# Kernel tuning notes

Measured on AMD Instinct MI355X. Metric: run time of the kernel, lower is better.

## Reference

```python
import jax, jax.numpy as jnp
import numpy as np

B, A, D, H, F = 256, 96, 384, 192, 96   # molecules, atoms, feat, hidden, species-MLP out
S = 4                                   # number of species (H, C, N, O)
E = B * A * 32                          # edges (avg degree 32)
CUTOFF = 5.2


def smooth_cutoff(d, cutoff):
    # Smoothstep-style cutoff: 1 at d=0, smoothly -> 0 at d=cutoff (Smoothstep class, reversed edges)
    x = jnp.clip((cutoff - d) / cutoff, 0.0, 1.0)
    return x ** 3 * (x * (6.0 * x - 15.0) + 10.0)


def setup_inputs() -> dict:
    key = jax.random.key(0)
    ks = jax.random.split(key, 9)
    species = jax.random.randint(ks[0], (B, A), 0, S, dtype=jnp.int32)
    in_features = jax.random.normal(ks[1], (B, A, D), dtype=jnp.float32)
    atom_index12 = jax.random.randint(ks[2], (2, E), 0, B * A, dtype=jnp.int32)
    distances = jax.random.uniform(ks[3], (E,), jnp.float32, 0.1, CUTOFF)
    total_charges = jnp.zeros((B,), jnp.float32)
    W1 = jax.random.normal(ks[4], (S, D, H), jnp.float32) / np.float32(np.sqrt(D))
    W2 = jax.random.normal(ks[5], (S, H, F), jnp.float32) / np.float32(np.sqrt(H))
    Wn = jax.random.normal(ks[6], (S, F, F), jnp.float32) / np.float32(np.sqrt(F))
    Wf = jax.random.normal(ks[7], (S, 2 * F, 1), jnp.float32) / np.float32(np.sqrt(2 * F))
    return dict(species=species, in_features=in_features, atom_index12=atom_index12,
                distances=distances, total_charges=total_charges,
                W1=W1, W2=W2, Wn=Wn, Wf=Wf,
                decay_prefactor=jnp.asarray(1.0, jnp.float32),
                decay_factor=jnp.asarray(1.0, jnp.float32))


def reference(species, in_features, atom_index12, distances, total_charges,
              W1, W2, Wn, Wf, decay_prefactor, decay_factor):
    b, a, d = in_features.shape
    n = b * a
    sp = species.reshape(-1)                      # [N]
    x = in_features.reshape(n, d)                 # [N, D]

    # per-species main MLP dispatch: internal[i] = MLP_{sp[i]}(x[i])
    internal = jnp.zeros((n, F), x.dtype)
    for s in range(S):
        mask = (sp == s)[:, None]
        h = jax.nn.gelu(x @ W1[s]) @ W2[s]        # [N, F]
        internal = internal + jnp.where(mask, h, jnp.zeros((), x.dtype))

    # per-species neighbor MLP
    nbr = jnp.zeros((n, F), x.dtype)
    for s in range(S):
        mask = (sp == s)[:, None]
        nbr = nbr + jnp.where(mask, internal @ Wn[s], jnp.zeros((), x.dtype))

    # distance-decayed edge messages: merged[i0] += nbr[i1]*w, merged[i1] += nbr[i0]*w
    decay = (decay_prefactor ** 2) * jnp.exp(-(decay_factor ** 2) * distances) \
            * smooth_cutoff(distances, CUTOFF)    # [E]
    i0, i1 = atom_index12[0], atom_index12[1]
    m_to_i0 = nbr[i1] * decay[:, None]            # [E, F]
    m_to_i1 = nbr[i0] * decay[:, None]
    merged = jax.ops.segment_sum(jnp.concatenate([m_to_i0, m_to_i1], axis=0),
                                 jnp.concatenate([i0, i1], axis=0),
                                 num_segments=n)  # [N, F]

    feats = jnp.concatenate([internal, merged], axis=-1)  # [N, 2F]

    # per-species final head -> precharges
    precharges = jnp.zeros((n,), x.dtype)
    for s in range(S):
        mask = (sp == s)
        precharges = precharges + jnp.where(mask, (feats @ Wf[s])[:, 0], jnp.zeros((), x.dtype))
    precharges = precharges.reshape(b, a)

    # total-charge redistribution (uniform factors, no learned redistribution)
    dummy_mask = species != -1
    factors = 1.0 / dummy_mask.sum(-1, keepdims=True).astype(x.dtype)
    charges = precharges + (total_charges - precharges.sum(-1))[:, None] * factors
    charges = jnp.where(dummy_mask, charges, jnp.zeros((), x.dtype))
    return species, charges, precharges
```

## Files before the change

### kernel.cpp

```cpp
#include <hip/hip_runtime.h>
#include <cstdint>
#include <cstddef>

#define NBm 256
#define NAm 96
#define NDm 384
#define NHm 192
#define NFm 96
#define NSm 4
#define NATOMS (NBm*NAm)
#define NEe (NATOMS*32)
#define NMSG (2*NEe)
#define HBLK 1536
#define CUTOFF_ 5.2f

typedef __attribute__((ext_vector_type(8))) short short8;
typedef __attribute__((ext_vector_type(4))) float float4v;
typedef __attribute__((ext_vector_type(2))) int int2v;

__device__ __forceinline__ short f2bf(float f){
  union { float f; unsigned u; } v; v.f = f;
  unsigned r = v.u + 0x7FFFu + ((v.u >> 16) & 1u);
  return (short)(r >> 16);
}

__device__ __forceinline__ float gelu_t(float x){
  float u = 0.7978845608028654f * (x + 0.044715f * x*x*x);
  float e = __expf(-2.0f * fabsf(u));
  float t = (1.0f - e) / (1.0f + e);
  t = (u >= 0.f) ? t : -t;
  return 0.5f * x * (1.0f + t);
}

__global__ void k_zero4(int* __restrict__ spc){
  if (threadIdx.x < NSm) spc[threadIdx.x] = 0;
}

__global__ void k_spcount(const int* __restrict__ sp, int* __restrict__ spc){
  __shared__ int h[NSm];
  int t = threadIdx.x;
  if (t < NSm) h[t] = 0;
  __syncthreads();
  int i = blockIdx.x*256 + t;
  atomicAdd(&h[sp[i]], 1);
  __syncthreads();
  if (t < NSm) atomicAdd(&spc[t], h[t]);
}

__global__ void k_spscan(const int* __restrict__ spc, int* __restrict__ sps, int* __restrict__ spcur){
  if (threadIdx.x==0 && blockIdx.x==0){
    int r=0;
    for (int s=0;s<NSm;s++){ sps[s]=r; spcur[s]=r; r+=spc[s]; }
    sps[NSm]=r;
  }
}

__global__ void k_spscatter(const int* __restrict__ sp, int* __restrict__ spcur,
                            int* __restrict__ order){
  __shared__ int h[NSm], base[NSm];
  int t = threadIdx.x;
  if (t < NSm) h[t]=0;
  __syncthreads();
  int i = blockIdx.x*256 + t;
  int s = sp[i];
  int lr = atomicAdd(&h[s], 1);
  __syncthreads();
  if (t < NSm) base[t] = atomicAdd(&spcur[t], h[t]);
  __syncthreads();
  order[base[s] + lr] = i;
}

#define W1N (NSm*NDm*NHm)
#define W2N (NSm*NHm*NFm)
#define WNN (NSm*NFm*NFm)
__global__ void k_wprep(const float* __restrict__ W1, const float* __restrict__ W2,
                        const float* __restrict__ Wn,
                        short* __restrict__ W1t, short* __restrict__ W2t,
                        short* __restrict__ Wnt){
  int idx = blockIdx.x*256 + threadIdx.x;
  if (idx < W1N){
    int s = idx / (NDm*NHm); int rem = idx - s*NDm*NHm;
    int k = rem / NHm, c = rem - k*NHm;
    W1t[(s*NHm + c)*NDm + k] = f2bf(W1[idx]);
  } else if (idx < W1N + W2N){
    int j = idx - W1N;
    int s = j / (NHm*NFm); int rem = j - s*NHm*NFm;
    int k = rem / NFm, c = rem - k*NFm;
    W2t[(s*NFm + c)*NHm + k] = f2bf(W2[j]);
  } else if (idx < W1N + W2N + WNN){
    int j = idx - W1N - W2N;
    int s = j / (NFm*NFm); int rem = j - s*NFm*NFm;
    int k = rem / NFm, c = rem - k*NFm;
    Wnt[(s*NFm + c)*NFm + k] = f2bf(Wn[j]);
  }
}

__global__ void k_xprep(const float* __restrict__ X, short* __restrict__ Xb){
  int i = (blockIdx.x*256 + threadIdx.x) * 8;
  float4v a = *(const float4v*)(X + i);
  float4v b = *(const float4v*)(X + i + 4);
  short8 o;
  o[0]=f2bf(a[0]); o[1]=f2bf(a[1]); o[2]=f2bf(a[2]); o[3]=f2bf(a[3]);
  o[4]=f2bf(b[0]); o[5]=f2bf(b[1]); o[6]=f2bf(b[2]); o[7]=f2bf(b[3]);
  *(short8*)(Xb + i) = o;
}

__global__ __launch_bounds__(256) void k_mlp(
    const short* __restrict__ Xb, const int* __restrict__ order,
    const int* __restrict__ sps,
    const short* __restrict__ W1t, const short* __restrict__ W2t,
    const short* __restrict__ Wnt,
    float* __restrict__ internal_g, float* __restrict__ nbr_g){
  const int s = blockIdx.y;
  const int s0 = sps[s];
  const int cnt = sps[s+1] - s0;
  const int row0 = blockIdx.x * 64;
  if (row0 >= cnt) return;

  __shared__ short Hs[64][200];
  __shared__ short Ws[192*40];
  __shared__ short Is[64][104];
  __shared__ int aids[64];

  const int tid = threadIdx.x;
  if (tid < 64){
    int r = row0 + tid;
    aids[tid] = order[s0 + ((r < cnt) ? r : 0)];
  }
  __syncthreads();

  const int wave = tid >> 6, lane = tid & 63;
  const int lrow = lane & 15, quad = lane >> 4;
  const int arow = wave*16 + lrow;
  const short* xrow = Xb + (size_t)aids[arow]*NDm + quad*8;

  short8 afs[12];
  #pragma unroll
  for (int kb=0; kb<12; kb++) afs[kb] = *(const short8*)(xrow + kb*32);

  const short* W1s = W1t + (size_t)s*NHm*NDm;
  float4v acc[12];
  #pragma unroll
  for (int i=0;i<12;i++){ acc[i][0]=0.f; acc[i][1]=0.f; acc[i][2]=0.f; acc[i][3]=0.f; }

  for (int kb=0; kb<12; kb++){
    __syncthreads();
    for (int e = tid; e < 192*4; e += 256){
      int c = e >> 2, kq = (e & 3) * 8;
      *(short8*)(&Ws[c*40 + kq]) = *(const short8*)(W1s + c*NDm + kb*32 + kq);
    }
    __syncthreads();
    short8 af = afs[kb];
    #pragma unroll
    for (int ct=0; ct<12; ct++){
      short8 bfb = *(const short8*)(&Ws[(ct*16 + lrow)*40 + quad*8]);
      acc[ct] = __builtin_amdgcn_mfma_f32_16x16x32_bf16(af, bfb, acc[ct], 0,0,0);
    }
  }
  #pragma unroll
  for (int ct=0; ct<12; ct++){
    #pragma unroll
    for (int r=0;r<4;r++){
      Hs[wave*16 + quad*4 + r][ct*16 + lrow] = f2bf(gelu_t(acc[ct][r]));
    }
  }

  const short* W2s = W2t + (size_t)s*NFm*NHm;
  float4v acc2[6];
  #pragma unroll
  for (int i=0;i<6;i++){ acc2[i][0]=0.f; acc2[i][1]=0.f; acc2[i][2]=0.f; acc2[i][3]=0.f; }
  for (int kb=0; kb<6; kb++){
    __syncthreads();
    for (int e = tid; e < 96*4; e += 256){
      int c = e >> 2, kq = (e & 3) * 8;
      *(short8*)(&Ws[c*40 + kq]) = *(const short8*)(W2s + c*NHm + kb*32 + kq);
    }
    __syncthreads();
    short8 af2 = *(const short8*)(&Hs[wave*16 + lrow][kb*32 + quad*8]);
    #pragma unroll
    for (int ct=0; ct<6; ct++){
      short8 bfb = *(const short8*)(&Ws[(ct*16 + lrow)*40 + quad*8]);
      acc2[ct] = __builtin_amdgcn_mfma_f32_16x16x32_bf16(af2, bfb, acc2[ct], 0,0,0);
    }
  }
  #pragma unroll
  for (int ct=0; ct<6; ct++){
    #pragma unroll
    for (int r=0;r<4;r++){
      int row = wave*16 + quad*4 + r, col = ct*16 + lrow;
      float v = acc2[ct][r];
      if (row0 + row < cnt) internal_g[(size_t)aids[row]*NFm + col] = v;
      Is[row][col] = f2bf(v);
    }
  }

  const short* Wns = Wnt + (size_t)s*NFm*NFm;
  float4v acc3[6];
  #pragma unroll
  for (int i=0;i<6;i++){ acc3[i][0]=0.f; acc3[i][1]=0.f; acc3[i][2]=0.f; acc3[i][3]=0.f; }
  for (int kb=0; kb<3; kb++){
    __syncthreads();
    for (int e = tid; e < 96*4; e += 256){
      int c = e >> 2, kq = (e & 3) * 8;
      *(short8*)(&Ws[c*40 + kq]) = *(const short8*)(Wns + c*NFm + kb*32 + kq);
    }
    __syncthreads();
    short8 af3 = *(const short8*)(&Is[wave*16 + lrow][kb*32 + quad*8]);
    #pragma unroll
    for (int ct=0; ct<6; ct++){
      short8 bfb = *(const short8*)(&Ws[(ct*16 + lrow)*40 + quad*8]);
      acc3[ct] = __builtin_amdgcn_mfma_f32_16x16x32_bf16(af3, bfb, acc3[ct], 0,0,0);
    }
  }
  #pragma unroll
  for (int ct=0; ct<6; ct++){
    #pragma unroll
    for (int r=0;r<4;r++){
      int row = wave*16 + quad*4 + r, col = ct*16 + lrow;
      if (row0 + row < cnt) nbr_g[(size_t)aids[row]*NFm + col] = acc3[ct][r];
    }
  }
}

__global__ void k_nd4(const float* __restrict__ internal, const float* __restrict__ nbr,
                      const int* __restrict__ sp, const float* __restrict__ Wf,
                      float* __restrict__ pre, float* __restrict__ nd4){
  int a = blockIdx.x*4 + (threadIdx.x >> 6);
  int lane = threadIdx.x & 63;
  bool lo = lane < 32;
  const float* ip = internal + (size_t)a*NFm;
  const float* np = nbr + (size_t)a*NFm;
  float iv1 = ip[lane],            nv1 = np[lane];
  float iv2 = lo ? ip[64+lane]:0.f, nv2 = lo ? np[64+lane]:0.f;
  int s = sp[a];
  const float* wfs = Wf + s*2*NFm;
  float d = iv1*wfs[lane] + (lo ? iv2*wfs[64+lane] : 0.f);
  float n0, n1, n2, n3;
  {
    const float* w0 = Wf + 0*2*NFm + NFm;
    const float* w1 = Wf + 1*2*NFm + NFm;
    const float* w2 = Wf + 2*2*NFm + NFm;
    const float* w3 = Wf + 3*2*NFm + NFm;
    n0 = nv1*w0[lane] + (lo ? nv2*w0[64+lane] : 0.f);
    n1 = nv1*w1[lane] + (lo ? nv2*w1[64+lane] : 0.f);
    n2 = nv1*w2[lane] + (lo ? nv2*w2[64+lane] : 0.f);
    n3 = nv1*w3[lane] + (lo ? nv2*w3[64+lane] : 0.f);
  }
  #pragma unroll
  for (int m=1; m<64; m<<=1){
    d  += __shfl_xor(d,  m, 64);
    n0 += __shfl_xor(n0, m, 64);
    n1 += __shfl_xor(n1, m, 64);
    n2 += __shfl_xor(n2, m, 64);
    n3 += __shfl_xor(n3, m, 64);
  }
  if (lane == 0){
    pre[a] = d;
    float4v v; v[0]=n0; v[1]=n1; v[2]=n2; v[3]=n3;
    *(float4v*)(nd4 + (size_t)a*4) = v;
  }
}

__global__ __launch_bounds__(1024) void k_hist(const int* __restrict__ ai,
                                               int* __restrict__ Hist){
  __shared__ int h[NBm];
  int t = threadIdx.x;
  if (t < NBm) h[t] = 0;
  __syncthreads();
  int m = blockIdx.x*1024 + t;
  int mol = ai[m] / NAm;
  atomicAdd(&h[mol], 1);
  __syncthreads();
  if (t < NBm) Hist[blockIdx.x*NBm + t] = h[t];
}

__global__ void k_mscan(int* __restrict__ Hist, int* __restrict__ Tot){
  __shared__ int sums[256];
  int mol = blockIdx.x, t = threadIdx.x;
  int v[6]; int loc = 0;
  #pragma unroll
  for (int j=0;j<6;j++){ v[j] = Hist[(t*6+j)*NBm + mol]; loc += v[j]; }
  sums[t] = loc; __syncthreads();
  for (int off=1; off<256; off<<=1){
    int x = (t >= off) ? sums[t-off] : 0;
    __syncthreads();
    sums[t] += x;
    __syncthreads();
  }
  int run = sums[t] - loc;
  #pragma unroll
  for (int j=0;j<6;j++){ Hist[(t*6+j)*NBm + mol] = run; run += v[j]; }
  if (t == 255) Tot[mol] = run;
}

__global__ void k_segscan(const int* __restrict__ Tot, int* __restrict__ Seg){
  __shared__ int s[256];
  int t = threadIdx.x;
  int v = Tot[t]; s[t] = v; __syncthreads();
  for (int off=1; off<256; off<<=1){
    int x = (t >= off) ? s[t-off] : 0;
    __syncthreads();
    s[t] += x;
    __syncthreads();
  }
  Seg[t] = s[t] - v;
  if (t == 255) Seg[256] = s[255];
}

__global__ __launch_bounds__(1024) void k_scatter(const int* __restrict__ ai,
    const float* __restrict__ dist, const float* __restrict__ pref,
    const float* __restrict__ fac, const int* __restrict__ Hist,
    const int* __restrict__ Seg, int2v* __restrict__ Msg){
  __shared__ int cnt[NBm];
  __shared__ int off[NBm];
  int t = threadIdx.x;
  if (t < NBm){ cnt[t] = 0; off[t] = Seg[t] + Hist[blockIdx.x*NBm + t]; }
  __syncthreads();
  int m = blockIdx.x*1024 + t;
  int dest = ai[m];
  int other = ai[(m < NEe) ? m + NEe : m - NEe];
  int e = (m < NEe) ? m : m - NEe;
  float d = dist[e];
  float x = (CUTOFF_ - d) * (1.0f/CUTOFF_);
  x = fminf(fmaxf(x, 0.f), 1.f);
  float sc = x*x*x*(x*(6.f*x - 15.f) + 10.f);
  float p = pref[0], fc = fac[0];
  float w = p*p * expf(-fc*fc*d) * sc;
  int mol = dest / NAm, dl = dest - mol*NAm;
  int rank = atomicAdd(&cnt[mol], 1);
  int2v msg; msg[0] = (other << 7) | dl; msg[1] = __float_as_int(w);
  Msg[off[mol] + rank] = msg;
}

__global__ __launch_bounds__(256) void k_accum(const int* __restrict__ Seg,
    const int2v* __restrict__ Msg, const float* __restrict__ nd4,
    const int* __restrict__ sp, const float* __restrict__ pre,
    const float* __restrict__ tc, float* __restrict__ out){
  __shared__ float acc[NAm];
  __shared__ int spl[NAm];
  __shared__ float red[128];
  int mol = blockIdx.x, t = threadIdx.x;
  if (t < NAm){ acc[t] = 0.f; spl[t] = sp[mol*NAm + t]; }
  __syncthreads();
  int s0 = Seg[mol], s1 = Seg[mol+1];
  for (int i = s0 + t; i < s1; i += 256){
    int2v kw = Msg[i];
    int key = kw[0]; float w = __int_as_float(kw[1]);
    int dl = key & 127, other = key >> 7;
    float val = w * nd4[(size_t)other*4 + spl[dl]];
    atomicAdd(&acc[dl], val);
  }
  __syncthreads();
  float pch = 0.f;
  if (t < NAm) pch = pre[mol*NAm + t] + acc[t];
  if (t < 128) red[t] = (t < NAm) ? pch : 0.f;
  __syncthreads();
  for (int o=64; o>0; o>>=1){
    if (t < o) red[t] += red[t + o];
    __syncthreads();
  }
  float sum = red[0];
  if (t < NAm){
    float c = pch + (tc[mol] - sum) * (1.0f/96.0f);
    out[mol*NAm + t] = (float)spl[t];
    out[NATOMS + mol*NAm + t] = c;
    out[2*NATOMS + mol*NAm + t] = pch;
  }
}

extern "C" void kernel_launch(void* const* d_in, const int* in_sizes, int n_in,
                              void* d_out, int out_size, void* d_ws, size_t ws_size,
                              hipStream_t stream) {
  const int*   species = (const int*)  d_in[0];
  const float* X       = (const float*)d_in[1];
  const int*   ai      = (const int*)  d_in[2];
  const float* dist    = (const float*)d_in[3];
  const float* tc      = (const float*)d_in[4];
  const float* W1      = (const float*)d_in[5];
  const float* W2      = (const float*)d_in[6];
  const float* Wn      = (const float*)d_in[7];
  const float* Wf      = (const float*)d_in[8];
  const float* pref    = (const float*)d_in[9];
  const float* fac     = (const float*)d_in[10];
  float* out = (float*)d_out;

  char* w = (char*)d_ws;
  auto alloc = [&](size_t bytes)->char*{
    char* p = w; w += (bytes + 255) & ~(size_t)255; return p;
  };
  int*   spc      = (int*)  alloc(64);
  int*   sps      = (int*)  alloc(64);
  int*   spcur    = (int*)  alloc(64);
  int*   order    = (int*)  alloc((size_t)NATOMS*4);
  float* nd4      = (float*)alloc((size_t)NATOMS*4*4);
  float* internal = (float*)alloc((size_t)NATOMS*NFm*4);
  float* nbr      = (float*)alloc((size_t)NATOMS*NFm*4);
  float* pre      = (float*)alloc((size_t)NATOMS*4);
  short* W1t      = (short*)alloc((size_t)W1N*2);
  short* W2t      = (short*)alloc((size_t)W2N*2);
  short* Wnt      = (short*)alloc((size_t)WNN*2);
  int*   Hist     = (int*)  alloc((size_t)HBLK*NBm*4);
  int*   Tot      = (int*)  alloc(1024);
  int*   Seg      = (int*)  alloc((NBm+1)*4);
  short* Xb       = (short*)alloc((size_t)NATOMS*NDm*2);
  int2v* Msg      = (int2v*)Xb;

  k_zero4<<<1, 64, 0, stream>>>(spc);
  k_wprep<<<(W1N+W2N+WNN)/256, 256, 0, stream>>>(W1, W2, Wn, W1t, W2t, Wnt);
  k_xprep<<<NATOMS*NDm/8/256, 256, 0, stream>>>(X, Xb);
  k_spcount<<<NATOMS/256, 256, 0, stream>>>(species, spc);
  k_spscan<<<1, 64, 0, stream>>>(spc, sps, spcur);
  k_spscatter<<<NATOMS/256, 256, 0, stream>>>(species, spcur, order);
  dim3 g(NATOMS/64, NSm);
  k_mlp<<<g, 256, 0, stream>>>(Xb, order, sps, W1t, W2t, Wnt, internal, nbr);
  k_nd4<<<NATOMS/4, 256, 0, stream>>>(internal, nbr, species, Wf, pre, nd4);
  k_hist<<<HBLK, 1024, 0, stream>>>(ai, Hist);
  k_mscan<<<NBm, 256, 0, stream>>>(Hist, Tot);
  k_segscan<<<1, 256, 0, stream>>>(Tot, Seg);
  k_scatter<<<HBLK, 1024, 0, stream>>>(ai, dist, pref, fac, Hist, Seg, Msg);
  k_accum<<<NBm, 256, 0, stream>>>(Seg, Msg, nd4, species, pre, tc, out);
}
```

Baseline: 203.1 us.

## Fuse bf16 input conversion and internal-head dot product into MLP kernel

The separate fp32-to-bf16 conversion pass over X is removed; the MLP kernel now loads fp32 rows and converts them in registers. The internal-feature half of the final head (dot with Wf) is computed inside the MLP kernel with a shuffle reduction, so the internal [N,F] fp32 tensor is no longer written or re-read. The zeroing kernel is folded into k_wprep, and Msg gets its own buffer instead of aliasing Xb. The tradeoff is scalar fp32 gathers (8 floats per k-block) in the MLP prologue instead of vector bf16 loads, which may raise load instruction count and register pressure.

```diff
diff --git a/kernel.cpp b/kernel.cpp
--- a/kernel.cpp
+++ b/kernel.cpp
@@ -32,51 +32,14 @@
   return 0.5f * x * (1.0f + t);
 }
 
-__global__ void k_zero4(int* __restrict__ spc){
-  if (threadIdx.x < NSm) spc[threadIdx.x] = 0;
-}
-
-__global__ void k_spcount(const int* __restrict__ sp, int* __restrict__ spc){
-  __shared__ int h[NSm];
-  int t = threadIdx.x;
-  if (t < NSm) h[t] = 0;
-  __syncthreads();
-  int i = blockIdx.x*256 + t;
-  atomicAdd(&h[sp[i]], 1);
-  __syncthreads();
-  if (t < NSm) atomicAdd(&spc[t], h[t]);
-}
-
-__global__ void k_spscan(const int* __restrict__ spc, int* __restrict__ sps, int* __restrict__ spcur){
-  if (threadIdx.x==0 && blockIdx.x==0){
-    int r=0;
-    for (int s=0;s<NSm;s++){ sps[s]=r; spcur[s]=r; r+=spc[s]; }
-    sps[NSm]=r;
-  }
-}
-
-__global__ void k_spscatter(const int* __restrict__ sp, int* __restrict__ spcur,
-                            int* __restrict__ order){
-  __shared__ int h[NSm], base[NSm];
-  int t = threadIdx.x;
-  if (t < NSm) h[t]=0;
-  __syncthreads();
-  int i = blockIdx.x*256 + t;
-  int s = sp[i];
-  int lr = atomicAdd(&h[s], 1);
-  __syncthreads();
-  if (t < NSm) base[t] = atomicAdd(&spcur[t], h[t]);
-  __syncthreads();
-  order[base[s] + lr] = i;
-}
-
 #define W1N (NSm*NDm*NHm)
 #define W2N (NSm*NHm*NFm)
 #define WNN (NSm*NFm*NFm)
 __global__ void k_wprep(const float* __restrict__ W1, const float* __restrict__ W2,
                         const float* __restrict__ Wn,
                         short* __restrict__ W1t, short* __restrict__ W2t,
-                        short* __restrict__ Wnt){
+                        short* __restrict__ Wnt, int* __restrict__ spc){
+  if (blockIdx.x == 0 && threadIdx.x < NSm) spc[threadIdx.x] = 0;
   int idx = blockIdx.x*256 + threadIdx.x;
   if (idx < W1N){
     int s = idx / (NDm*NHm); int rem = idx - s*NDm*NHm;
@@ -95,22 +58,46 @@
   }
 }
 
-__global__ void k_xprep(const float* __restrict__ X, short* __restrict__ Xb){
-  int i = (blockIdx.x*256 + threadIdx.x) * 8;
-  float4v a = *(const float4v*)(X + i);
-  float4v b = *(const float4v*)(X + i + 4);
-  short8 o;
-  o[0]=f2bf(a[0]); o[1]=f2bf(a[1]); o[2]=f2bf(a[2]); o[3]=f2bf(a[3]);
-  o[4]=f2bf(b[0]); o[5]=f2bf(b[1]); o[6]=f2bf(b[2]); o[7]=f2bf(b[3]);
-  *(short8*)(Xb + i) = o;
+__global__ void k_spcount(const int* __restrict__ sp, int* __restrict__ spc){
+  __shared__ int h[NSm];
+  int t = threadIdx.x;
+  if (t < NSm) h[t] = 0;
+  __syncthreads();
+  int i = blockIdx.x*256 + t;
+  atomicAdd(&h[sp[i]], 1);
+  __syncthreads();
+  if (t < NSm) atomicAdd(&spc[t], h[t]);
+}
+
+__global__ void k_spscan(const int* __restrict__ spc, int* __restrict__ sps, int* __restrict__ spcur){
+  if (threadIdx.x==0 && blockIdx.x==0){
+    int r=0;
+    for (int s=0;s<NSm;s++){ sps[s]=r; spcur[s]=r; r+=spc[s]; }
+    sps[NSm]=r;
+  }
+}
+
+__global__ void k_spscatter(const int* __restrict__ sp, int* __restrict__ spcur,
+                            int* __restrict__ order){
+  __shared__ int h[NSm], base[NSm];
+  int t = threadIdx.x;
+  if (t < NSm) h[t]=0;
+  __syncthreads();
+  int i = blockIdx.x*256 + t;
+  int s = sp[i];
+  int lr = atomicAdd(&h[s], 1);
+  __syncthreads();
+  if (t < NSm) base[t] = atomicAdd(&spcur[t], h[t]);
+  __syncthreads();
+  order[base[s] + lr] = i;
 }
 
 __global__ __launch_bounds__(256) void k_mlp(
-    const short* __restrict__ Xb, const int* __restrict__ order,
+    const float* __restrict__ X, const int* __restrict__ order,
     const int* __restrict__ sps,
     const short* __restrict__ W1t, const short* __restrict__ W2t,
-    const short* __restrict__ Wnt,
-    float* __restrict__ internal_g, float* __restrict__ nbr_g){
+    const short* __restrict__ Wnt, const float* __restrict__ Wf,
+    float* __restrict__ pre, float* __restrict__ nbr_g){
   const int s = blockIdx.y;
   const int s0 = sps[s];
   const int cnt = sps[s+1] - s0;
@@ -132,11 +119,15 @@
   const int wave = tid >> 6, lane = tid & 63;
   const int lrow = lane & 15, quad = lane >> 4;
   const int arow = wave*16 + lrow;
-  const short* xrow = Xb + (size_t)aids[arow]*NDm + quad*8;
+  const float* xrow = X + (size_t)aids[arow]*NDm + quad*8;
 
   short8 afs[12];
   #pragma unroll
-  for (int kb=0; kb<12; kb++) afs[kb] = *(const short8*)(xrow + kb*32);
+  for (int kb=0; kb<12; kb++){
+    const float* p = xrow + kb*32;
+    #pragma unroll
+    for (int j=0;j<8;j++) afs[kb][j] = f2bf(p[j]);
+  }
 
   const short* W1s = W1t + (size_t)s*NHm*NDm;
   float4v acc[12];
@@ -187,10 +178,29 @@
   for (int ct=0; ct<6; ct++){
     #pragma unroll
     for (int r=0;r<4;r++){
-      int row = wave*16 + quad*4 + r, col = ct*16 + lrow;
-      float v = acc2[ct][r];
-      if (row0 + row < cnt) internal_g[(size_t)aids[row]*NFm + col] = v;
-      Is[row][col] = f2bf(v);
+      Is[wave*16 + quad*4 + r][ct*16 + lrow] = f2bf(acc2[ct][r]);
+    }
+  }
+
+  {
+    float pr[4] = {0.f,0.f,0.f,0.f};
+    #pragma unroll
+    for (int ct=0; ct<6; ct++){
+      float wv = Wf[s*2*NFm + ct*16 + lrow];
+      #pragma unroll
+      for (int r=0;r<4;r++) pr[r] += acc2[ct][r] * wv;
+    }
+    #pragma unroll
+    for (int m=1; m<16; m<<=1){
+      #pragma unroll
+      for (int r=0;r<4;r++) pr[r] += __shfl_xor(pr[r], m, 64);
+    }
+    if (lrow == 0){
+      #pragma unroll
+      for (int r=0;r<4;r++){
+        int row = wave*16 + quad*4 + r;
+        if (row0 + row < cnt) pre[aids[row]] = pr[r];
+      }
     }
   }
 
@@ -222,40 +232,30 @@
   }
 }
 
-__global__ void k_nd4(const float* __restrict__ internal, const float* __restrict__ nbr,
-                      const int* __restrict__ sp, const float* __restrict__ Wf,
-                      float* __restrict__ pre, float* __restrict__ nd4){
+__global__ void k_nd4(const float* __restrict__ nbr, const float* __restrict__ Wf,
+                      float* __restrict__ nd4){
   int a = blockIdx.x*4 + (threadIdx.x >> 6);
   int lane = threadIdx.x & 63;
   bool lo = lane < 32;
-  const float* ip = internal + (size_t)a*NFm;
   const float* np = nbr + (size_t)a*NFm;
-  float iv1 = ip[lane],            nv1 = np[lane];
-  float iv2 = lo ? ip[64+lane]:0.f, nv2 = lo ? np[64+lane]:0.f;
-  int s = sp[a];
-  const float* wfs = Wf + s*2*NFm;
-  float d = iv1*wfs[lane] + (lo ? iv2*wfs[64+lane] : 0.f);
-  float n0, n1, n2, n3;
-  {
-    const float* w0 = Wf + 0*2*NFm + NFm;
-    const float* w1 = Wf + 1*2*NFm + NFm;
-    const float* w2 = Wf + 2*2*NFm + NFm;
-    const float* w3 = Wf + 3*2*NFm + NFm;
-    n0 = nv1*w0[lane] + (lo ? nv2*w0[64+lane] : 0.f);
-    n1 = nv1*w1[lane] + (lo ? nv2*w1[64+lane] : 0.f);
-    n2 = nv1*w2[lane] + (lo ? nv2*w2[64+lane] : 0.f);
-    n3 = nv1*w3[lane] + (lo ? nv2*w3[64+lane] : 0.f);
-  }
+  float nv1 = np[lane];
+  float nv2 = lo ? np[64+lane] : 0.f;
+  const float* w0 = Wf + 0*2*NFm + NFm;
+  const float* w1 = Wf + 1*2*NFm + NFm;
+  const float* w2 = Wf + 2*2*NFm + NFm;
+  const float* w3 = Wf + 3*2*NFm + NFm;
+  float n0 = nv1*w0[lane] + (lo ? nv2*w0[64+lane] : 0.f);
+  float n1 = nv1*w1[lane] + (lo ? nv2*w1[64+lane] : 0.f);
+  float n2 = nv1*w2[lane] + (lo ? nv2*w2[64+lane] : 0.f);
+  float n3 = nv1*w3[lane] + (lo ? nv2*w3[64+lane] : 0.f);
   #pragma unroll
   for (int m=1; m<64; m<<=1){
-    d  += __shfl_xor(d,  m, 64);
     n0 += __shfl_xor(n0, m, 64);
     n1 += __shfl_xor(n1, m, 64);
     n2 += __shfl_xor(n2, m, 64);
     n3 += __shfl_xor(n3, m, 64);
   }
   if (lane == 0){
-    pre[a] = d;
     float4v v; v[0]=n0; v[1]=n1; v[2]=n2; v[3]=n3;
     *(float4v*)(nd4 + (size_t)a*4) = v;
   }
@@ -388,32 +388,28 @@
   auto alloc = [&](size_t bytes)->char*{
     char* p = w; w += (bytes + 255) & ~(size_t)255; return p;
   };
-  int*   spc      = (int*)  alloc(64);
-  int*   sps      = (int*)  alloc(64);
-  int*   spcur    = (int*)  alloc(64);
-  int*   order    = (int*)  alloc((size_t)NATOMS*4);
-  float* nd4      = (float*)alloc((size_t)NATOMS*4*4);
-  float* internal = (float*)alloc((size_t)NATOMS*NFm*4);
-  float* nbr      = (float*)alloc((size_t)NATOMS*NFm*4);
-  float* pre      = (float*)alloc((size_t)NATOMS*4);
-  short* W1t      = (short*)alloc((size_t)W1N*2);
-  short* W2t      = (short*)alloc((size_t)W2N*2);
-  short* Wnt      = (short*)alloc((size_t)WNN*2);
-  int*   Hist     = (int*)  alloc((size_t)HBLK*NBm*4);
-  int*   Tot      = (int*)  alloc(1024);
-  int*   Seg      = (int*)  alloc((NBm+1)*4);
-  short* Xb       = (short*)alloc((size_t)NATOMS*NDm*2);
-  int2v* Msg      = (int2v*)Xb;
-
-  k_zero4<<<1, 64, 0, stream>>>(spc);
-  k_wprep<<<(W1N+W2N+WNN)/256, 256, 0, stream>>>(W1, W2, Wn, W1t, W2t, Wnt);
-  k_xprep<<<NATOMS*NDm/8/256, 256, 0, stream>>>(X, Xb);
+  int*   spc   = (int*)  alloc(64);
+  int*   sps   = (int*)  alloc(64);
+  int*   spcur = (int*)  alloc(64);
+  int*   order = (int*)  alloc((size_t)NATOMS*4);
+  float* nd4   = (float*)alloc((size_t)NATOMS*4*4);
+  float* pre   = (float*)alloc((size_t)NATOMS*4);
+  float* nbr   = (float*)alloc((size_t)NATOMS*NFm*4);
+  short* W1t   = (short*)alloc((size_t)W1N*2);
+  short* W2t   = (short*)alloc((size_t)W2N*2);
+  short* Wnt   = (short*)alloc((size_t)WNN*2);
+  int*   Hist  = (int*)  alloc((size_t)HBLK*NBm*4);
+  int*   Tot   = (int*)  alloc(1024);
+  int*   Seg   = (int*)  alloc((NBm+1)*4);
+  int2v* Msg   = (int2v*)alloc((size_t)NMSG*8);
+
+  k_wprep<<<(W1N+W2N+WNN)/256, 256, 0, stream>>>(W1, W2, Wn, W1t, W2t, Wnt, spc);
   k_spcount<<<NATOMS/256, 256, 0, stream>>>(species, spc);
   k_spscan<<<1, 64, 0, stream>>>(spc, sps, spcur);
   k_spscatter<<<NATOMS/256, 256, 0, stream>>>(species, spcur, order);
   dim3 g(NATOMS/64, NSm);
-  k_mlp<<<g, 256, 0, stream>>>(Xb, order, sps, W1t, W2t, Wnt, internal, nbr);
-  k_nd4<<<NATOMS/4, 256, 0, stream>>>(internal, nbr, species, Wf, pre, nd4);
+  k_mlp<<<g, 256, 0, stream>>>(X, order, sps, W1t, W2t, Wnt, Wf, pre, nbr);
+  k_nd4<<<NATOMS/4, 256, 0, stream>>>(nbr, Wf, nd4);
   k_hist<<<HBLK, 1024, 0, stream>>>(ai, Hist);
   k_mscan<<<NBm, 256, 0, stream>>>(Hist, Tot);
   k_segscan<<<1, 256, 0, stream>>>(Tot, Seg);
```

New measurement: 190.9 us. 6.0% less time.
